# Optimization experiments

Hardware: AMD Instinct MI355X
Metric: run time of the kernel (lower is better)

The kernel has to match this reference:

```python
import jax, jax.numpy as jnp
import numpy as np
from jax import lax

B, N_PARAMS, N_LAYERS = 8, 4, 5
CIN, COUT, K, MID = 64, 64, 3, 64
H, W = 256, 256
LAYER_IDX = 2
PAD = (K - 1) // 2  # 'preserve' padding, stride=1


def setup_inputs() -> dict:
    key = jax.random.key(0)
    ks = jax.random.split(key, 16)
    s = 0.002  # embedder init scale (xavier_normal_(x, 0.002) ~ tiny weights)
    inp = {
        "x": jax.random.normal(ks[0], (B, CIN, H, W), jnp.float32),
        "h": jax.random.normal(ks[1], (B, N_PARAMS), jnp.float32),
        "index": jnp.zeros((N_LAYERS,), jnp.float32).at[LAYER_IDX].set(1.0),
        "conv_weight": jax.random.normal(ks[2], (COUT, CIN, K, K), jnp.float32) * 0.05,
        "conv_bias": jax.random.normal(ks[3], (COUT,), jnp.float32) * 0.05,
        "W_wp": jax.random.normal(ks[4], (MID * CIN, N_PARAMS), jnp.float32) * s,
        "b_wp": jnp.zeros((MID * CIN,), jnp.float32),
        "W_wi": jax.random.normal(ks[5], (MID * CIN, N_LAYERS), jnp.float32) * s,
        "b_wi": jnp.zeros((MID * CIN,), jnp.float32),
        "W_we": jax.random.normal(ks[6], (COUT * K * K, MID), jnp.float32) * s,
        "b_we": jnp.zeros((COUT * K * K,), jnp.float32),
        "W_bp": jax.random.normal(ks[7], (COUT, N_PARAMS), jnp.float32) * s,
        "b_bp": jnp.zeros((COUT,), jnp.float32),
        "W_bi": jax.random.normal(ks[8], (COUT, N_LAYERS), jnp.float32) * s,
        "b_bi": jnp.zeros((COUT,), jnp.float32),
    }
    return inp


def _embed(h, index, W_wp, b_wp, W_wi, b_wi, W_we, b_we, W_bp, b_bp, W_bi, b_bi):
    # fc_w_param(h) + fc_w_index(index): (B, mid*in)
    w = h @ W_wp.T + b_wp + index @ W_wi.T + b_wi
    w = w.reshape(-1, CIN, MID)                      # (B, in, mid)
    w = w @ W_we.T + b_we                            # (B, in, out*k*k)
    w = w.reshape(-1, CIN, COUT, K, K).swapaxes(1, 2)  # (B, out, in, k, k)
    b = h @ W_bp.T + b_bp + index @ W_bi.T + b_bi    # (B, out)
    return w, b


def reference(x, h, index, conv_weight, conv_bias,
              W_wp, b_wp, W_wi, b_wi, W_we, b_we,
              W_bp, b_bp, W_bi, b_bi):
    dw, db = _embed(h, index, W_wp, b_wp, W_wi, b_wi, W_we, b_we,
                    W_bp, b_bp, W_bi, b_bi)
    weights = conv_weight[None] + dw           # (B, out, in, k, k)
    bias = conv_bias[None] + db                # (B, out)

    def conv_one(xi, wi):
        # xi: (in, H, W), wi: (out, in, k, k) -> (out, H, W)
        y = lax.conv_general_dilated(
            xi[None], wi, window_strides=(1, 1),
            padding=((PAD, PAD), (PAD, PAD)),
            dimension_numbers=("NCHW", "OIHW", "NCHW"))
        return y[0]

    y = jax.vmap(conv_one)(x, weights)         # per-sample weights == batch-as-groups conv
    return y + bias[:, :, None, None]
```

## Files before the change

kernel.cpp:

```cpp
#include <hip/hip_runtime.h>
#include <hip/hip_bf16.h>
#include <string.h>

typedef short  short8  __attribute__((ext_vector_type(8)));
typedef float  f32x16  __attribute__((ext_vector_type(16)));
typedef unsigned short ushort_t;

#define B_    8
#define CIN_  64
#define COUT_ 64
#define MID_  64
#define HH    256
#define WW    256
#define NP_   4
#define NL_   5

#define TR 8
#define TC 30
#define SR 10
#define SC 32
#define NJT 9
#define SLAB_ELE (SR*8*SC*8)
#define W_ELE    (9*8*COUT_*8)

__global__ __launch_bounds__(256)
void build_weights(const float* __restrict__ h, const float* __restrict__ index,
                   const float* __restrict__ conv_weight,
                   const float* __restrict__ W_wp, const float* __restrict__ b_wp,
                   const float* __restrict__ W_wi, const float* __restrict__ b_wi,
                   const float* __restrict__ W_we, const float* __restrict__ b_we,
                   ushort_t* __restrict__ wsW) {
    const int bb  = blockIdx.x >> 5;
    const int cig = blockIdx.x & 31;
    const int ci0 = cig * 2;
    const int tid = threadIdx.x;

    __shared__ float s_pre[2 * MID_];

    if (tid < 128) {
        const int cil = tid >> 6, mid = tid & 63;
        const int m = (ci0 + cil) * MID_ + mid;
        float acc = b_wp[m] + b_wi[m];
#pragma unroll
        for (int p = 0; p < NP_; ++p) acc += h[bb * NP_ + p] * W_wp[m * NP_ + p];
#pragma unroll
        for (int l = 0; l < NL_; ++l) acc += index[l] * W_wi[m * NL_ + l];
        s_pre[tid] = acc;
    }
    __syncthreads();

    for (int t = tid; t < 2 * 576; t += 256) {
        const int cil = t / 576;
        const int o9  = t - cil * 576;
        const float* wr = W_we + o9 * MID_;
        const float* pr = s_pre + cil * MID_;
        float a0 = b_we[o9], a1 = 0.f, a2 = 0.f, a3 = 0.f;
#pragma unroll 4
        for (int mid = 0; mid < MID_; mid += 4) {
            a0 += pr[mid]     * wr[mid];
            a1 += pr[mid + 1] * wr[mid + 1];
            a2 += pr[mid + 2] * wr[mid + 2];
            a3 += pr[mid + 3] * wr[mid + 3];
        }
        float acc = (a0 + a1) + (a2 + a3);
        const int co = o9 / 9;
        const int r  = o9 - co * 9;
        const int ci = ci0 + cil;
        acc += conv_weight[(co * CIN_ + ci) * 9 + r];
        __hip_bfloat16 hb = __float2bfloat16(acc);
        ushort_t bits; __builtin_memcpy(&bits, &hb, 2);
        wsW[(((bb * 9 + r) * 8 + (ci >> 3)) * COUT_ + co) * 8 + (ci & 7)] = bits;
    }
}

__device__ __forceinline__ void stage_slab(const float* __restrict__ xb, int i0, int j0,
                                           ushort_t* __restrict__ sl, int t,
                                           int rr0, int rr1) {
    const int c  = t & 31;
    const int pp = t >> 5;
    const int gc = j0 - 1 + c;
    const bool cok = (unsigned)gc < (unsigned)WW;
    const int gcc = cok ? gc : 0;
    unsigned int* sb = (unsigned int*)sl;
    for (int rr = rr0; rr < rr1; ++rr) {
        const int grow = i0 - 1 + rr;
        if ((unsigned)grow < (unsigned)HH) {
            const float* xr = xb + grow * WW + gcc;
#pragma unroll
            for (int it = 0; it < 4; ++it) {
                const int P = it * 8 + pp;
                float f0 = xr[(P * 2)     * (HH * WW)];
                float f1 = xr[(P * 2 + 1) * (HH * WW)];
                f0 = cok ? f0 : 0.f;
                f1 = cok ? f1 : 0.f;
                __hip_bfloat162 h2 = __float22bfloat162_rn(make_float2(f0, f1));
                unsigned int u; __builtin_memcpy(&u, &h2, 4);
                sb[((rr * 8 + (P >> 2)) * 32 + c) * 4 + (P & 3)] = u;
            }
        } else {
#pragma unroll
            for (int it = 0; it < 4; ++it) {
                const int P = it * 8 + pp;
                sb[((rr * 8 + (P >> 2)) * 32 + c) * 4 + (P & 3)] = 0u;
            }
        }
    }
}

__global__ __launch_bounds__(512)
void hyperconv(const float* __restrict__ x, const ushort_t* __restrict__ wsW,
               const float* __restrict__ conv_bias,
               const float* __restrict__ h, const float* __restrict__ index,
               const float* __restrict__ W_bp, const float* __restrict__ b_bp,
               const float* __restrict__ W_bi, const float* __restrict__ b_bi,
               float* __restrict__ out) {
    __shared__ __align__(16) ushort_t Wl[W_ELE];
    __shared__ __align__(16) ushort_t Sx[2][SLAB_ELE];
    __shared__ float biasl[COUT_];

    const int tid   = threadIdx.x;
    const int bb    = blockIdx.x >> 5;
    const int strip = blockIdx.x & 31;
    const int i0    = strip * TR;
    const float* xb = x + bb * CIN_ * HH * WW;

    {
        const uint4* src = (const uint4*)(wsW + bb * W_ELE);
        uint4* dst = (uint4*)Wl;
        for (int i = tid; i < W_ELE / 8; i += 512) dst[i] = src[i];
    }
    if (tid < COUT_) {
        const int co = tid;
        float a = conv_bias[co] + b_bp[co] + b_bi[co];
#pragma unroll
        for (int p = 0; p < NP_; ++p) a += h[bb * NP_ + p] * W_bp[co * NP_ + p];
#pragma unroll
        for (int l = 0; l < NL_; ++l) a += index[l] * W_bi[co * NL_ + l];
        biasl[co] = a;
    }
    stage_slab(xb, i0, 0, &Sx[0][0], tid & 255, (tid >> 8) * 5, (tid >> 8) * 5 + 5);

    const int lane = tid & 63;
    const int wv   = tid >> 6;
    const int n    = lane & 31;
    const int hl   = lane >> 5;
    int q[2], cc[2]; bool dead[2];
#pragma unroll
    for (int d = 0; d < 2; ++d) {
        const int flat = (2 * wv + d) * 32 + n;
        int qq = flat / 30;
        const int c2 = flat - qq * 30;
        dead[d] = (flat >= 240);
        if (qq > 7) qq = 7;
        q[d] = qq; cc[d] = c2;
    }
    const int baseA  = hl * 512 + n * 8;
    const int baseB0 = q[0] * 2048 + hl * 256 + cc[0] * 8;
    const int baseB1 = q[1] * 2048 + hl * 256 + cc[1] * 8;

    __syncthreads();

    for (int jt = 0; jt < NJT; ++jt) {
        const int buf = jt & 1;
        if (tid >= 256) {
            if (jt + 1 < NJT)
                stage_slab(xb, i0, (jt + 1) * TC, &Sx[1 - buf][0], tid - 256, 0, SR);
        } else {
            const int j0 = jt * TC;
            const ushort_t* sl = &Sx[buf][0];
            f32x16 a00 = {}, a10 = {}, a01 = {}, a11 = {};
#pragma unroll
            for (int kh = 0; kh < 3; ++kh)
#pragma unroll
                for (int kw = 0; kw < 3; ++kw) {
                    const int khkw = kh * 3 + kw;
#pragma unroll
                    for (int kk = 0; kk < 4; ++kk) {
                        short8 A0 = *(const short8*)&Wl[baseA + khkw * 4096 + kk * 1024];
                        short8 A1 = *(const short8*)&Wl[baseA + khkw * 4096 + kk * 1024 + 256];
                        short8 Bf0 = *(const short8*)&sl[baseB0 + kh * 2048 + kw * 8 + kk * 512];
                        short8 Bf1 = *(const short8*)&sl[baseB1 + kh * 2048 + kw * 8 + kk * 512];
                        a00 = __builtin_amdgcn_mfma_f32_32x32x16_bf16(A0, Bf0, a00, 0, 0, 0);
                        a10 = __builtin_amdgcn_mfma_f32_32x32x16_bf16(A1, Bf0, a10, 0, 0, 0);
                        a01 = __builtin_amdgcn_mfma_f32_32x32x16_bf16(A0, Bf1, a01, 0, 0, 0);
                        a11 = __builtin_amdgcn_mfma_f32_32x32x16_bf16(A1, Bf1, a11, 0, 0, 0);
                    }
                }
#pragma unroll
            for (int d = 0; d < 2; ++d) {
                const f32x16& accL = d ? a01 : a00;
                const f32x16& accH = d ? a11 : a10;
                const bool valid = !dead[d] && (j0 + cc[d] < WW);
                if (valid) {
                    const int row  = i0 + q[d];
                    const int colg = j0 + cc[d];
                    float* op = out + (bb * COUT_) * (HH * WW) + row * WW + colg;
#pragma unroll
                    for (int r = 0; r < 16; ++r) {
                        const int coL = (r & 3) + 8 * (r >> 2) + 4 * hl;
                        op[coL * (HH * WW)] = accL[r] + biasl[coL];
                    }
#pragma unroll
                    for (int r = 0; r < 16; ++r) {
                        const int coH = (r & 3) + 8 * (r >> 2) + 4 * hl + 32;
                        op[coH * (HH * WW)] = accH[r] + biasl[coH];
                    }
                }
            }
        }
        __syncthreads();
    }
}

extern "C" void kernel_launch(void* const* d_in, const int* in_sizes, int n_in,
                              void* d_out, int out_size, void* d_ws, size_t ws_size,
                              hipStream_t stream) {
    const float* x           = (const float*)d_in[0];
    const float* h           = (const float*)d_in[1];
    const float* index       = (const float*)d_in[2];
    const float* conv_weight = (const float*)d_in[3];
    const float* conv_bias   = (const float*)d_in[4];
    const float* W_wp        = (const float*)d_in[5];
    const float* b_wp        = (const float*)d_in[6];
    const float* W_wi        = (const float*)d_in[7];
    const float* b_wi        = (const float*)d_in[8];
    const float* W_we        = (const float*)d_in[9];
    const float* b_we        = (const float*)d_in[10];
    const float* W_bp        = (const float*)d_in[11];
    const float* b_bp        = (const float*)d_in[12];
    const float* W_bi        = (const float*)d_in[13];
    const float* b_bi        = (const float*)d_in[14];

    float* out = (float*)d_out;
    ushort_t* wsW = (ushort_t*)d_ws;

    build_weights<<<256, 256, 0, stream>>>(
        h, index, conv_weight, W_wp, b_wp, W_wi, b_wi, W_we, b_we, wsW);

    hyperconv<<<256, 512, 0, stream>>>(
        x, wsW, conv_bias, h, index, W_bp, b_bp, W_bi, b_bi, out);
}
```

Measured before the change: 358.2 us.

## Register-prefetch input tiles, use all waves for MFMA, tile 32 columns

The conv kernel stops splitting the block into 256 producer and 256 consumer threads. All 8 waves now compute one output row each over 32-column tiles (8 tiles instead of 9, with no dead lanes), and the next tile is prefetched into registers while the current one computes. The weight-build kernel is rewritten to compute 64-output chunks per block using shared-memory staged W_we and pre-activations, with 72 blocks. This trades the double-buffered LDS slab for a single slab plus more registers per thread, and adds launch_bounds occupancy 2.

```diff
diff --git a/kernel.cpp b/kernel.cpp
--- a/kernel.cpp
+++ b/kernel.cpp
@@ -1,6 +1,5 @@
 #include <hip/hip_runtime.h>
 #include <hip/hip_bf16.h>
-#include <string.h>
 
 typedef short  short8  __attribute__((ext_vector_type(8)));
 typedef float  f32x16  __attribute__((ext_vector_type(16)));
@@ -16,12 +15,13 @@
 #define NL_   5
 
 #define TR 8
-#define TC 30
+#define TC 32
+#define NJT 8
 #define SR 10
-#define SC 32
-#define NJT 9
-#define SLAB_ELE (SR*8*SC*8)
-#define W_ELE    (9*8*COUT_*8)
+#define SCC 34
+#define SLAB_U32 (SR*8*SCC*4)
+#define W_SHORTS (9*8*COUT_*8)
+#define NSTG 22
 
 __global__ __launch_bounds__(256)
 void build_weights(const float* __restrict__ h, const float* __restrict__ index,
@@ -30,92 +30,101 @@
                    const float* __restrict__ W_wi, const float* __restrict__ b_wi,
                    const float* __restrict__ W_we, const float* __restrict__ b_we,
                    ushort_t* __restrict__ wsW) {
-    const int bb  = blockIdx.x >> 5;
-    const int cig = blockIdx.x & 31;
-    const int ci0 = cig * 2;
+    const int bb  = blockIdx.x / 9;
+    const int ch  = blockIdx.x - bb * 9;
     const int tid = threadIdx.x;
 
-    __shared__ float s_pre[2 * MID_];
-
-    if (tid < 128) {
-        const int cil = tid >> 6, mid = tid & 63;
-        const int m = (ci0 + cil) * MID_ + mid;
-        float acc = b_wp[m] + b_wi[m];
-#pragma unroll
-        for (int p = 0; p < NP_; ++p) acc += h[bb * NP_ + p] * W_wp[m * NP_ + p];
-#pragma unroll
-        for (int l = 0; l < NL_; ++l) acc += index[l] * W_wi[m * NL_ + l];
-        s_pre[tid] = acc;
+    __shared__ float pre_s[64 * 66];
+    __shared__ float chunk_s[64 * 64];
+
+    float hv[NP_], iv[NL_];
+#pragma unroll
+    for (int p = 0; p < NP_; ++p) hv[p] = h[bb * NP_ + p];
+#pragma unroll
+    for (int l = 0; l < NL_; ++l) iv[l] = index[l];
+
+#pragma unroll
+    for (int k = 0; k < 16; ++k) {
+        const int m = tid + k * 256;
+        float a = b_wp[m] + b_wi[m];
+#pragma unroll
+        for (int p = 0; p < NP_; ++p) a += hv[p] * W_wp[m * NP_ + p];
+#pragma unroll
+        for (int l = 0; l < NL_; ++l) a += iv[l] * W_wi[m * NL_ + l];
+        pre_s[(m >> 6) * 66 + (m & 63)] = a;
+    }
+#pragma unroll
+    for (int k = 0; k < 16; ++k) {
+        const int f = tid + k * 256;
+        chunk_s[f] = W_we[ch * 4096 + f];
     }
     __syncthreads();
 
-    for (int t = tid; t < 2 * 576; t += 256) {
-        const int cil = t / 576;
-        const int o9  = t - cil * 576;
-        const float* wr = W_we + o9 * MID_;
-        const float* pr = s_pre + cil * MID_;
-        float a0 = b_we[o9], a1 = 0.f, a2 = 0.f, a3 = 0.f;
-#pragma unroll 4
-        for (int mid = 0; mid < MID_; mid += 4) {
-            a0 += pr[mid]     * wr[mid];
-            a1 += pr[mid + 1] * wr[mid + 1];
-            a2 += pr[mid + 2] * wr[mid + 2];
-            a3 += pr[mid + 3] * wr[mid + 3];
-        }
-        float acc = (a0 + a1) + (a2 + a3);
+    const int ci = tid & 63;
+    const int g  = tid >> 6;
+    float acc[16];
+#pragma unroll
+    for (int u = 0; u < 16; ++u) acc[u] = 0.f;
+
+#pragma unroll
+    for (int mid = 0; mid < 64; mid += 2) {
+        const float2 pv = *(const float2*)&pre_s[ci * 66 + mid];
+#pragma unroll
+        for (int u = 0; u < 16; ++u) {
+            const float2 wv = *(const float2*)&chunk_s[(g + 4 * u) * 64 + mid];
+            acc[u] += pv.x * wv.x + pv.y * wv.y;
+        }
+    }
+
+#pragma unroll
+    for (int u = 0; u < 16; ++u) {
+        const int o9 = ch * 64 + g + 4 * u;
         const int co = o9 / 9;
         const int r  = o9 - co * 9;
-        const int ci = ci0 + cil;
-        acc += conv_weight[(co * CIN_ + ci) * 9 + r];
-        __hip_bfloat16 hb = __float2bfloat16(acc);
+        const float val = acc[u] + b_we[o9] + conv_weight[(co * CIN_ + ci) * 9 + r];
+        __hip_bfloat16 hb = __float2bfloat16(val);
         ushort_t bits; __builtin_memcpy(&bits, &hb, 2);
         wsW[(((bb * 9 + r) * 8 + (ci >> 3)) * COUT_ + co) * 8 + (ci & 7)] = bits;
     }
 }
 
-__device__ __forceinline__ void stage_slab(const float* __restrict__ xb, int i0, int j0,
-                                           ushort_t* __restrict__ sl, int t,
-                                           int rr0, int rr1) {
-    const int c  = t & 31;
-    const int pp = t >> 5;
-    const int gc = j0 - 1 + c;
-    const bool cok = (unsigned)gc < (unsigned)WW;
-    const int gcc = cok ? gc : 0;
-    unsigned int* sb = (unsigned int*)sl;
-    for (int rr = rr0; rr < rr1; ++rr) {
-        const int grow = i0 - 1 + rr;
-        if ((unsigned)grow < (unsigned)HH) {
-            const float* xr = xb + grow * WW + gcc;
-#pragma unroll
-            for (int it = 0; it < 4; ++it) {
-                const int P = it * 8 + pp;
-                float f0 = xr[(P * 2)     * (HH * WW)];
-                float f1 = xr[(P * 2 + 1) * (HH * WW)];
-                f0 = cok ? f0 : 0.f;
-                f1 = cok ? f1 : 0.f;
-                __hip_bfloat162 h2 = __float22bfloat162_rn(make_float2(f0, f1));
-                unsigned int u; __builtin_memcpy(&u, &h2, 4);
-                sb[((rr * 8 + (P >> 2)) * 32 + c) * 4 + (P & 3)] = u;
-            }
-        } else {
-#pragma unroll
-            for (int it = 0; it < 4; ++it) {
-                const int P = it * 8 + pp;
-                sb[((rr * 8 + (P >> 2)) * 32 + c) * 4 + (P & 3)] = 0u;
-            }
-        }
-    }
-}
-
-__global__ __launch_bounds__(512)
+__device__ __forceinline__ void load_tile(const float* __restrict__ xb, int i0, int j0,
+                                          int tid, unsigned (&vals)[NSTG]) {
+#pragma unroll
+    for (int k = 0; k < NSTG; ++k) {
+        const int s = tid + k * 512;
+        unsigned v = 0u;
+        if (s < SLAB_U32) {
+            const int p  = s & 3;
+            const int t2 = s >> 2;
+            const int c  = t2 % SCC;
+            const int t3 = t2 / SCC;
+            const int g  = t3 & 7;
+            const int r  = t3 >> 3;
+            const int gr = i0 - 1 + r;
+            const int gc = j0 - 1 + c;
+            const int ci = g * 8 + p * 2;
+            const bool ok = ((unsigned)gr < (unsigned)HH) && ((unsigned)gc < (unsigned)WW);
+            const float* px = xb + ci * (HH * WW) + (ok ? (gr * WW + gc) : 0);
+            float f0 = px[0];
+            float f1 = px[HH * WW];
+            if (!ok) { f0 = 0.f; f1 = 0.f; }
+            const __hip_bfloat162 h2 = __float22bfloat162_rn(make_float2(f0, f1));
+            __builtin_memcpy(&v, &h2, 4);
+        }
+        vals[k] = v;
+    }
+}
+
+__global__ __launch_bounds__(512, 2)
 void hyperconv(const float* __restrict__ x, const ushort_t* __restrict__ wsW,
                const float* __restrict__ conv_bias,
                const float* __restrict__ h, const float* __restrict__ index,
                const float* __restrict__ W_bp, const float* __restrict__ b_bp,
                const float* __restrict__ W_bi, const float* __restrict__ b_bi,
                float* __restrict__ out) {
-    __shared__ __align__(16) ushort_t Wl[W_ELE];
-    __shared__ __align__(16) ushort_t Sx[2][SLAB_ELE];
+    __shared__ __align__(16) ushort_t Wl[W_SHORTS];
+    __shared__ __align__(16) unsigned Slab[SLAB_U32];
     __shared__ float biasl[COUT_];
 
     const int tid   = threadIdx.x;
@@ -124,10 +133,13 @@
     const int i0    = strip * TR;
     const float* xb = x + bb * CIN_ * HH * WW;
 
+    unsigned vals[NSTG];
+    load_tile(xb, i0, 0, tid, vals);
+
     {
-        const uint4* src = (const uint4*)(wsW + bb * W_ELE);
+        const uint4* src = (const uint4*)(wsW + bb * W_SHORTS);
         uint4* dst = (uint4*)Wl;
-        for (int i = tid; i < W_ELE / 8; i += 512) dst[i] = src[i];
+        for (int i = tid; i < W_SHORTS / 8; i += 512) dst[i] = src[i];
     }
     if (tid < COUT_) {
         const int co = tid;
@@ -138,77 +150,53 @@
         for (int l = 0; l < NL_; ++l) a += index[l] * W_bi[co * NL_ + l];
         biasl[co] = a;
     }
-    stage_slab(xb, i0, 0, &Sx[0][0], tid & 255, (tid >> 8) * 5, (tid >> 8) * 5 + 5);
 
     const int lane = tid & 63;
     const int wv   = tid >> 6;
     const int n    = lane & 31;
     const int hl   = lane >> 5;
-    int q[2], cc[2]; bool dead[2];
-#pragma unroll
-    for (int d = 0; d < 2; ++d) {
-        const int flat = (2 * wv + d) * 32 + n;
-        int qq = flat / 30;
-        const int c2 = flat - qq * 30;
-        dead[d] = (flat >= 240);
-        if (qq > 7) qq = 7;
-        q[d] = qq; cc[d] = c2;
-    }
-    const int baseA  = hl * 512 + n * 8;
-    const int baseB0 = q[0] * 2048 + hl * 256 + cc[0] * 8;
-    const int baseB1 = q[1] * 2048 + hl * 256 + cc[1] * 8;
-
-    __syncthreads();
 
     for (int jt = 0; jt < NJT; ++jt) {
-        const int buf = jt & 1;
-        if (tid >= 256) {
-            if (jt + 1 < NJT)
-                stage_slab(xb, i0, (jt + 1) * TC, &Sx[1 - buf][0], tid - 256, 0, SR);
-        } else {
-            const int j0 = jt * TC;
-            const ushort_t* sl = &Sx[buf][0];
-            f32x16 a00 = {}, a10 = {}, a01 = {}, a11 = {};
-#pragma unroll
-            for (int kh = 0; kh < 3; ++kh)
-#pragma unroll
-                for (int kw = 0; kw < 3; ++kw) {
-                    const int khkw = kh * 3 + kw;
-#pragma unroll
-                    for (int kk = 0; kk < 4; ++kk) {
-                        short8 A0 = *(const short8*)&Wl[baseA + khkw * 4096 + kk * 1024];
-                        short8 A1 = *(const short8*)&Wl[baseA + khkw * 4096 + kk * 1024 + 256];
-                        short8 Bf0 = *(const short8*)&sl[baseB0 + kh * 2048 + kw * 8 + kk * 512];
-                        short8 Bf1 = *(const short8*)&sl[baseB1 + kh * 2048 + kw * 8 + kk * 512];
-                        a00 = __builtin_amdgcn_mfma_f32_32x32x16_bf16(A0, Bf0, a00, 0, 0, 0);
-                        a10 = __builtin_amdgcn_mfma_f32_32x32x16_bf16(A1, Bf0, a10, 0, 0, 0);
-                        a01 = __builtin_amdgcn_mfma_f32_32x32x16_bf16(A0, Bf1, a01, 0, 0, 0);
-                        a11 = __builtin_amdgcn_mfma_f32_32x32x16_bf16(A1, Bf1, a11, 0, 0, 0);
-                    }
-                }
-#pragma unroll
-            for (int d = 0; d < 2; ++d) {
-                const f32x16& accL = d ? a01 : a00;
-                const f32x16& accH = d ? a11 : a10;
-                const bool valid = !dead[d] && (j0 + cc[d] < WW);
-                if (valid) {
-                    const int row  = i0 + q[d];
-                    const int colg = j0 + cc[d];
-                    float* op = out + (bb * COUT_) * (HH * WW) + row * WW + colg;
-#pragma unroll
-                    for (int r = 0; r < 16; ++r) {
-                        const int coL = (r & 3) + 8 * (r >> 2) + 4 * hl;
-                        op[coL * (HH * WW)] = accL[r] + biasl[coL];
-                    }
-#pragma unroll
-                    for (int r = 0; r < 16; ++r) {
-                        const int coH = (r & 3) + 8 * (r >> 2) + 4 * hl + 32;
-                        op[coH * (HH * WW)] = accH[r] + biasl[coH];
-                    }
+        __syncthreads();
+#pragma unroll
+        for (int k = 0; k < NSTG; ++k) {
+            const int s = tid + k * 512;
+            if (s < SLAB_U32) Slab[s] = vals[k];
+        }
+        if (jt + 1 < NJT) load_tile(xb, i0, (jt + 1) * TC, tid, vals);
+        __syncthreads();
+
+        f32x16 a0 = {}, a1 = {};
+        const ushort_t* sl = (const ushort_t*)Slab;
+#pragma unroll
+        for (int kh = 0; kh < 3; ++kh)
+#pragma unroll
+            for (int kw = 0; kw < 3; ++kw) {
+                const int khkw = kh * 3 + kw;
+#pragma unroll
+                for (int kk = 0; kk < 4; ++kk) {
+                    const int gA = khkw * 8 + 2 * kk + hl;
+                    const short8 A0 = *(const short8*)&Wl[(gA * 64 + n) * 8];
+                    const short8 A1 = *(const short8*)&Wl[(gA * 64 + n + 32) * 8];
+                    const int gB = ((wv + kh) * 8 + 2 * kk + hl) * SCC + (n + kw);
+                    const short8 Bf = *(const short8*)&sl[gB * 8];
+                    a0 = __builtin_amdgcn_mfma_f32_32x32x16_bf16(A0, Bf, a0, 0, 0, 0);
+                    a1 = __builtin_amdgcn_mfma_f32_32x32x16_bf16(A1, Bf, a1, 0, 0, 0);
                 }
             }
-        }
-        __syncthreads();
+
+        const int j0 = jt * TC;
+        float* op = out + (size_t)(bb * COUT_) * (HH * WW) + (i0 + wv) * WW + j0 + n;
+#pragma unroll
+        for (int r = 0; r < 16; ++r) {
+            const int co = (r & 3) + 8 * (r >> 2) + 4 * hl;
+            op[co * (HH * WW)] = a0[r] + biasl[co];
+        }
+#pragma unroll
+        for (int r = 0; r < 16; ++r) {
+            const int co = (r & 3) + 8 * (r >> 2) + 4 * hl + 32;
+            op[co * (HH * WW)] = a1[r] + biasl[co];
+        }
     }
 }
 
@@ -234,7 +222,7 @@
     float* out = (float*)d_out;
     ushort_t* wsW = (ushort_t*)d_ws;
 
-    build_weights<<<256, 256, 0, stream>>>(
+    build_weights<<<72, 256, 0, stream>>>(
         h, index, conv_weight, W_wp, b_wp, W_wi, b_wi, W_we, b_we, wsW);
 
     hyperconv<<<256, 512, 0, stream>>>(
```

Result: faster. 330.5 us (-7.7%).
